# Performance work log

Hardware: AMD Instinct MI355X
Metric: run time of the kernel (lower is better)

Reference implementation:

```python
import jax, jax.numpy as jnp
import numpy as np

N_HEADS = 8
D_HEAD = 64
INNER = N_HEADS * D_HEAD  # 512
D_X = 512
D_CTX = 768

def setup_inputs() -> dict:
    key = jax.random.key(0)
    ks = jax.random.split(key, 7)
    x = jax.random.normal(ks[0], (4, 4096, D_X), dtype=jnp.float32)
    context = jax.random.normal(ks[1], (4, 1024, D_CTX), dtype=jnp.float32)
    # Glorot-ish scaled params
    Wq = jax.random.normal(ks[2], (D_X, INNER), dtype=jnp.float32) / np.sqrt(D_X)
    Wk = jax.random.normal(ks[3], (D_CTX, INNER), dtype=jnp.float32) / np.sqrt(D_CTX)
    Wv = jax.random.normal(ks[4], (D_CTX, INNER), dtype=jnp.float32) / np.sqrt(D_CTX)
    Wo = jax.random.normal(ks[5], (INNER, INNER), dtype=jnp.float32) / np.sqrt(INNER)
    bo = jnp.zeros((INNER,), dtype=jnp.float32)
    return {"x": x, "context": context, "Wq": Wq, "Wk": Wk, "Wv": Wv, "Wo": Wo, "bo": bo}

def reference(x, context, Wq, Wk, Wv, Wo, bo):
    B, Nq, _ = x.shape
    Nc = context.shape[1]
    scale = D_HEAD ** -0.5
    # QKV projections (no bias), reshape to heads: b s (h d) -> b h s d
    q = (x @ Wq).reshape(B, Nq, N_HEADS, D_HEAD).transpose(0, 2, 1, 3)
    k = (context @ Wk).reshape(B, Nc, N_HEADS, D_HEAD).transpose(0, 2, 1, 3)
    v = (context @ Wv).reshape(B, Nc, N_HEADS, D_HEAD).transpose(0, 2, 1, 3)
    # scores: [B, H, Nq, Nc]
    score = jnp.einsum('bhqd,bhkd->bhqk', q, k) * scale
    weights = jax.nn.softmax(score, axis=-1)
    attn = jnp.einsum('bhqk,bhkd->bhqd', weights, v)
    out = attn.transpose(0, 2, 1, 3).reshape(B, Nq, INNER)
    return out @ Wo + bo
```

## Files before the change

### kernel.cpp

```cpp
#include <hip/hip_runtime.h>
#include <math.h>

typedef __attribute__((ext_vector_type(8))) short s8v;
typedef __attribute__((ext_vector_type(4))) float f4v;
typedef unsigned short u16;
typedef unsigned int u32;

constexpr int Bsz = 4, NQ = 4096, NC = 1024, NH = 8, DH = 64, DI = 512, DC = 768;

__device__ __forceinline__ u16 f2bf(float f) {
  union { float f; u32 u; } v; v.f = f;
  u32 r = v.u + 0x7fff + ((v.u >> 16) & 1);
  return (u16)(r >> 16);
}

__device__ __forceinline__ u32 pack2(float a, float b) {
  union { float f; u32 u; } ua, ub; ua.f = a; ub.f = b;
#if __has_builtin(__builtin_amdgcn_perm)
  return __builtin_amdgcn_perm(ub.u + 0x8000u, ua.u + 0x8000u, 0x07060302u);
#else
  return ((ub.u + 0x8000u) & 0xffff0000u) | ((ua.u + 0x8000u) >> 16);
#endif
}

#if __has_builtin(__builtin_amdgcn_exp2f)
#define EXP2(x) __builtin_amdgcn_exp2f(x)
#else
#define EXP2(x) exp2f(x)
#endif

__device__ __forceinline__ void g2l16(const void* g, void* l) {
  __builtin_amdgcn_global_load_lds((const __attribute__((address_space(1))) u32*)g,
                                   (__attribute__((address_space(3))) u32*)l, 16, 0, 0);
}

__global__ __launch_bounds__(256) void prep(const float* __restrict__ x, const float* __restrict__ ctx,
                                            const float* __restrict__ Wq, const float* __restrict__ Wk,
                                            const float* __restrict__ Wv, const float* __restrict__ Wo,
                                            u16* __restrict__ xb, u16* __restrict__ cb,
                                            u16* __restrict__ wqT, u16* __restrict__ wkvT,
                                            u16* __restrict__ woT) {
  int bx = blockIdx.x;
  if (bx < 11264) {
    const int NX4 = Bsz * NQ * DI / 4;
    const int NC4 = Bsz * NC * DC / 4;
    int i = bx * 256 + threadIdx.x;
    float4 v; u16* dst; int j;
    if (i < NX4) { v = ((const float4*)x)[i]; dst = xb; j = i; }
    else { j = i - NX4; if (j >= NC4) return; v = ((const float4*)ctx)[j]; dst = cb; }
    ushort4 o; o.x = f2bf(v.x); o.y = f2bf(v.y); o.z = f2bf(v.z); o.w = f2bf(v.w);
    ((ushort4*)dst)[j] = o;
    return;
  }
  int idx = bx - 11264;
  int z = idx / 96, rem = idx % 96, kx = rem % 12, ny = rem / 12;
  const float* src; u16* dst; int K; const int N = 512;
  if (z == 0)      { src = Wq; dst = wqT;              K = 512; }
  else if (z == 1) { src = Wk; dst = wkvT;             K = 768; }
  else if (z == 2) { src = Wv; dst = wkvT + 512 * 768; K = 768; }
  else             { src = Wo; dst = woT;              K = 512; }
  int k0 = kx * 64, n0 = ny * 64;
  if (k0 >= K) return;
  __shared__ u16 t[64][65];
  int tid = threadIdx.x, jr = tid & 63, ir = tid >> 6;
  for (int it = 0; it < 16; ++it) { int i = it * 4 + ir; t[i][jr] = f2bf(src[(size_t)(k0 + i) * N + n0 + jr]); }
  __syncthreads();
  for (int it = 0; it < 16; ++it) { int i = it * 4 + ir; dst[(size_t)(n0 + i) * K + k0 + jr] = t[jr][i]; }
}

template <int MODE>
__device__ __forceinline__ void gemm_body(const u16* __restrict__ A, const u16* __restrict__ Bt,
                                          void* __restrict__ C0, void* __restrict__ C1,
                                          const float* __restrict__ bias, int N, int K,
                                          float oscale, int nbx, int mby,
                                          u16* Al, u16* Bl) {
  int mb = mby * 128, nb = nbx * 64;
  int tid = threadIdx.x, lane = tid & 63, quad = lane >> 4, l16 = lane & 15, wave = tid >> 6;
  int wm = (wave >> 1) * 64, wn = (wave & 1) * 32;
  f4v acc[4][2];
  #pragma unroll
  for (int i = 0; i < 4; i++)
    #pragma unroll
    for (int j = 0; j < 2; j++) acc[i][j] = (f4v){0.f, 0.f, 0.f, 0.f};

  int r0 = tid >> 2, c0 = (tid & 3) * 8;
  const u16* Ap0 = A + (size_t)(mb + r0) * K + c0;
  const u16* Ap1 = A + (size_t)(mb + r0 + 64) * K + c0;
  const u16* Bp0 = Bt + (size_t)(nb + r0) * K + c0;

#define GSTAGE(k0, buf) do { \
    u16* al_ = Al + (buf) * 4096; u16* bl_ = Bl + (buf) * 2048; \
    g2l16(Ap0 + (k0), al_ + tid * 8); \
    g2l16(Ap1 + (k0), al_ + (tid + 256) * 8); \
    g2l16(Bp0 + (k0), bl_ + tid * 8); } while (0)

  GSTAGE(0, 0);
  int nk = K >> 5;
  for (int t = 0; t < nk; ++t) {
    __syncthreads();
    if (t + 1 < nk) GSTAGE((t + 1) * 32, (t + 1) & 1);
    const u16* al = Al + (t & 1) * 4096;
    const u16* bl = Bl + (t & 1) * 2048;
    s8v af[4], bfr[2];
    #pragma unroll
    for (int i = 0; i < 4; i++) af[i] = *(const s8v*)(al + (wm + i * 16 + l16) * 32 + quad * 8);
    #pragma unroll
    for (int j = 0; j < 2; j++) bfr[j] = *(const s8v*)(bl + (wn + j * 16 + l16) * 32 + quad * 8);
    #pragma unroll
    for (int i = 0; i < 4; i++)
      #pragma unroll
      for (int j = 0; j < 2; j++)
        acc[i][j] = __builtin_amdgcn_mfma_f32_16x16x32_bf16(af[i], bfr[j], acc[i][j], 0, 0, 0);
  }
#undef GSTAGE
  #pragma unroll
  for (int i = 0; i < 4; i++) {
    int rbase = mb + wm + i * 16 + quad * 4;
    #pragma unroll
    for (int j = 0; j < 2; j++) {
      int col = nb + wn + j * 16 + l16;
      if (MODE == 0) {
        u16* Cb = (u16*)C0;
        #pragma unroll
        for (int r = 0; r < 4; r++) Cb[(size_t)(rbase + r) * N + col] = f2bf(acc[i][j][r] * oscale);
      } else if (MODE == 1) {
        float* Cf = (float*)C0;
        #pragma unroll
        for (int r = 0; r < 4; r++) Cf[(size_t)(rbase + r) * N + col] = acc[i][j][r] + bias[col];
      } else {
        if (nbx < 8) {
          u16* Kb = (u16*)C0;
          #pragma unroll
          for (int r = 0; r < 4; r++) Kb[(size_t)(rbase + r) * 512 + col] = f2bf(acc[i][j][r]);
        } else {
          u16* Vt = (u16*)C1;
          int hd = col - 512, h = hd >> 6, d = hd & 63;
          int bb = rbase >> 10, tl = rbase & 1023;
          int tbase = tl & ~63, a0 = tl & 63;
          int pb = (a0 & 32) + ((a0 & 15) >> 2) * 8 + (((a0 >> 4) & 1) << 2);
          uint2 ov;
          ov.x = pack2(acc[i][j][0], acc[i][j][1]);
          ov.y = pack2(acc[i][j][2], acc[i][j][3]);
          *(uint2*)(Vt + ((size_t)(bb * NH + h) * DH + d) * NC + tbase + pb) = ov;
        }
      }
    }
  }
}

__global__ __launch_bounds__(256, 4) void proj_all(const u16* __restrict__ xb, const u16* __restrict__ cb,
                                                   const u16* __restrict__ wqT, const u16* __restrict__ wkvT,
                                                   u16* __restrict__ Qb, u16* __restrict__ Kb,
                                                   u16* __restrict__ Vtb, float qscale) {
  __shared__ alignas(16) u16 Al[2][128][32];
  __shared__ alignas(16) u16 Bl[2][64][32];
  int bx = blockIdx.x;
  if (bx < 1024) {
    gemm_body<0>(xb, wqT, Qb, nullptr, nullptr, 512, 512, qscale, bx & 7, bx >> 3,
                 (u16*)Al, (u16*)Bl);
  } else {
    int bi = bx - 1024;
    gemm_body<2>(cb, wkvT, Kb, Vtb, nullptr, 1024, 768, 1.0f, bi & 15, bi >> 4,
                 (u16*)Al, (u16*)Bl);
  }
}

__global__ __launch_bounds__(256, 4) void outproj(const u16* __restrict__ Ob, const u16* __restrict__ woT,
                                                  float* __restrict__ out, const float* __restrict__ bo) {
  __shared__ alignas(16) u16 Al[2][128][32];
  __shared__ alignas(16) u16 Bl[2][64][32];
  gemm_body<1>(Ob, woT, out, nullptr, bo, 512, 512, 1.0f, blockIdx.x, blockIdx.y,
               (u16*)Al, (u16*)Bl);
}

__global__ __launch_bounds__(128, 2) void attn(const u16* __restrict__ Q, const u16* __restrict__ Kb,
                                               const u16* __restrict__ Vt, u16* __restrict__ O) {
  __shared__ alignas(16) u16 Kl[2][64][64];
  __shared__ alignas(16) u16 Vl[2][64][64];
  int qt = blockIdx.x, h = blockIdx.y, b = blockIdx.z;
  int tid = threadIdx.x, wave = tid >> 6, lane = tid & 63, quad = lane >> 4, l16 = lane & 15;
  int q0 = qt * 128 + wave * 64;
  int x7 = l16 & 7;

  int kr = tid >> 3, kc = (tid & 7) ^ (kr & 7);
  const u16* kg = Kb + ((size_t)b * NC + kr) * 512 + h * DH + kc * 8;
  const u16* vg = Vt + ((size_t)(b * NH + h) * DH + kr) * NC + kc * 8;

#define ASTAGE(kt, buf) do { \
    const u16* kg_ = kg + (size_t)(kt) * 64 * 512; \
    const u16* vg_ = vg + (kt) * 64; \
    u16* kl_ = (u16*)Kl + (buf) * 4096; u16* vl_ = (u16*)Vl + (buf) * 4096; \
    _Pragma("unroll") \
    for (int it = 0; it < 4; ++it) { \
      g2l16(kg_ + (size_t)it * 16 * 512, kl_ + (tid + it * 128) * 8); \
      g2l16(vg_ + (size_t)it * 16 * NC,  vl_ + (tid + it * 128) * 8); \
    } } while (0)

  s8v aq[4][2];
  {
    const u16* Qp = Q + ((size_t)b * NQ + q0 + l16) * DI + h * DH + quad * 8;
    #pragma unroll
    for (int n = 0; n < 4; n++) {
      aq[n][0] = *(const s8v*)(Qp + (size_t)n * 16 * DI);
      aq[n][1] = *(const s8v*)(Qp + (size_t)n * 16 * DI + 32);
    }
  }
  f4v oacc[4][4];
  float lsum[4] = {0.f, 0.f, 0.f, 0.f};
  #pragma unroll
  for (int d = 0; d < 4; d++)
    #pragma unroll
    for (int n = 0; n < 4; n++) oacc[d][n] = (f4v){0.f, 0.f, 0.f, 0.f};

  ASTAGE(0, 0);
  for (int kt = 0; kt < NC / 64; ++kt) {
    int buf = kt & 1;
    __syncthreads();
    if (kt + 1 < NC / 64) ASTAGE(kt + 1, buf ^ 1);
    const u16* kb = (const u16*)Kl + buf * 4096;
    const u16* vb = (const u16*)Vl + buf * 4096;

    #pragma unroll
    for (int c = 0; c < 2; c++) {
      f4v S[2][4];
      #pragma unroll
      for (int mi = 0; mi < 2; mi++)
        #pragma unroll
        for (int n = 0; n < 4; n++) S[mi][n] = (f4v){0.f, 0.f, 0.f, 0.f};
      #pragma unroll
      for (int cd = 0; cd < 2; cd++) {
        int rA = 32 * c + l16;
        int ch = ((4 * cd + quad) ^ x7) * 8;
        s8v kf0 = *(const s8v*)(kb + rA * 64 + ch);
        s8v kf1 = *(const s8v*)(kb + (rA + 16) * 64 + ch);
        #pragma unroll
        for (int n = 0; n < 4; n++) {
          S[0][n] = __builtin_amdgcn_mfma_f32_16x16x32_bf16(kf0, aq[n][cd], S[0][n], 0, 0, 0);
          S[1][n] = __builtin_amdgcn_mfma_f32_16x16x32_bf16(kf1, aq[n][cd], S[1][n], 0, 0, 0);
        }
      }
      s8v pf[4];
      #pragma unroll
      for (int n = 0; n < 4; n++) {
        float p00 = EXP2(S[0][n][0]), p01 = EXP2(S[0][n][1]), p02 = EXP2(S[0][n][2]), p03 = EXP2(S[0][n][3]);
        float p10 = EXP2(S[1][n][0]), p11 = EXP2(S[1][n][1]), p12 = EXP2(S[1][n][2]), p13 = EXP2(S[1][n][3]);
        lsum[n] += (p00 + p01) + (p02 + p03) + (p10 + p11) + (p12 + p13);
        union { u32 d[4]; s8v v; } u;
        u.d[0] = pack2(p00, p01); u.d[1] = pack2(p02, p03);
        u.d[2] = pack2(p10, p11); u.d[3] = pack2(p12, p13);
        pf[n] = u.v;
      }
      #pragma unroll
      for (int d = 0; d < 4; d++) {
        int rV = d * 16 + l16;
        int ch = ((4 * c + quad) ^ x7) * 8;
        s8v vf = *(const s8v*)(vb + rV * 64 + ch);
        #pragma unroll
        for (int n = 0; n < 4; n++)
          oacc[d][n] = __builtin_amdgcn_mfma_f32_16x16x32_bf16(vf, pf[n], oacc[d][n], 0, 0, 0);
      }
    }
  }
#undef ASTAGE

  float inv[4];
  #pragma unroll
  for (int n = 0; n < 4; n++) {
    float s = lsum[n];
    s += __shfl_xor(s, 16); s += __shfl_xor(s, 32);
    inv[n] = 1.0f / s;
  }
  #pragma unroll
  for (int d = 0; d < 4; d++)
    #pragma unroll
    for (int n = 0; n < 4; n++) {
      int q = q0 + n * 16 + l16;
      uint2 ov;
      ov.x = pack2(oacc[d][n][0] * inv[n], oacc[d][n][1] * inv[n]);
      ov.y = pack2(oacc[d][n][2] * inv[n], oacc[d][n][3] * inv[n]);
      *(uint2*)(O + ((size_t)b * NQ + q) * DI + h * DH + d * 16 + quad * 4) = ov;
    }
}

extern "C" void kernel_launch(void* const* d_in, const int* in_sizes, int n_in,
                              void* d_out, int out_size, void* d_ws, size_t ws_size,
                              hipStream_t stream) {
  const float* x   = (const float*)d_in[0];
  const float* ctx = (const float*)d_in[1];
  const float* Wq  = (const float*)d_in[2];
  const float* Wk  = (const float*)d_in[3];
  const float* Wv  = (const float*)d_in[4];
  const float* Wo  = (const float*)d_in[5];
  const float* bo  = (const float*)d_in[6];
  float* out = (float*)d_out;

  u16* w    = (u16*)d_ws;
  u16* xb   = w;
  u16* cb   = xb   + 8388608;
  u16* wqT  = cb   + 3145728;
  u16* wkvT = wqT  + 262144;
  u16* woT  = wkvT + 786432;
  u16* Qb   = woT  + 262144;
  u16* Kbuf = Qb   + 8388608;
  u16* Vtb  = Kbuf + 2097152;
  u16* Ob   = Vtb  + 2097152;

  const float qscale = 0.125f * 1.44269504f;

  prep<<<11648, 256, 0, stream>>>(x, ctx, Wq, Wk, Wv, Wo, xb, cb, wqT, wkvT, woT);
  proj_all<<<1536, 256, 0, stream>>>(xb, cb, wqT, wkvT, Qb, Kbuf, Vtb, qscale);
  attn<<<dim3(32, 8, 4), 128, 0, stream>>>(Qb, Kbuf, Vtb, Ob);
  outproj<<<dim3(8, 128), 256, 0, stream>>>(Ob, woT, out, bo);
}
```

Baseline: 207.5 us.

## Widen projection GEMM tiles to 128x128 and shrink attention KV tiles to 32

The shared GEMM body now computes 128x128 output tiles, with each wave holding a 64x64 accumulator block. This halves the block count for the projection and output GEMMs and increases operand reuse per LDS load. The attention kernel streams K/V in 32-key tiles instead of 64, which halves its shared memory per block and raises the occupancy hint from 2 to 4 blocks per CU. The trade-offs are more accumulator registers and lower occupancy in the GEMMs, and twice as many barriers and load iterations in the attention loop.

```diff
diff --git a/kernel.cpp b/kernel.cpp
--- a/kernel.cpp
+++ b/kernel.cpp
@@ -74,25 +74,27 @@
                                           const float* __restrict__ bias, int N, int K,
                                           float oscale, int nbx, int mby,
                                           u16* Al, u16* Bl) {
-  int mb = mby * 128, nb = nbx * 64;
+  int mb = mby * 128, nb = nbx * 128;
   int tid = threadIdx.x, lane = tid & 63, quad = lane >> 4, l16 = lane & 15, wave = tid >> 6;
-  int wm = (wave >> 1) * 64, wn = (wave & 1) * 32;
-  f4v acc[4][2];
+  int wm = (wave >> 1) * 64, wn = (wave & 1) * 64;
+  f4v acc[4][4];
   #pragma unroll
   for (int i = 0; i < 4; i++)
     #pragma unroll
-    for (int j = 0; j < 2; j++) acc[i][j] = (f4v){0.f, 0.f, 0.f, 0.f};
+    for (int j = 0; j < 4; j++) acc[i][j] = (f4v){0.f, 0.f, 0.f, 0.f};
 
   int r0 = tid >> 2, c0 = (tid & 3) * 8;
   const u16* Ap0 = A + (size_t)(mb + r0) * K + c0;
   const u16* Ap1 = A + (size_t)(mb + r0 + 64) * K + c0;
   const u16* Bp0 = Bt + (size_t)(nb + r0) * K + c0;
+  const u16* Bp1 = Bt + (size_t)(nb + r0 + 64) * K + c0;
 
 #define GSTAGE(k0, buf) do { \
-    u16* al_ = Al + (buf) * 4096; u16* bl_ = Bl + (buf) * 2048; \
+    u16* al_ = Al + (buf) * 4096; u16* bl_ = Bl + (buf) * 4096; \
     g2l16(Ap0 + (k0), al_ + tid * 8); \
     g2l16(Ap1 + (k0), al_ + (tid + 256) * 8); \
-    g2l16(Bp0 + (k0), bl_ + tid * 8); } while (0)
+    g2l16(Bp0 + (k0), bl_ + tid * 8); \
+    g2l16(Bp1 + (k0), bl_ + (tid + 256) * 8); } while (0)
 
   GSTAGE(0, 0);
   int nk = K >> 5;
@@ -100,16 +102,16 @@
     __syncthreads();
     if (t + 1 < nk) GSTAGE((t + 1) * 32, (t + 1) & 1);
     const u16* al = Al + (t & 1) * 4096;
-    const u16* bl = Bl + (t & 1) * 2048;
-    s8v af[4], bfr[2];
+    const u16* bl = Bl + (t & 1) * 4096;
+    s8v af[4], bfr[4];
     #pragma unroll
     for (int i = 0; i < 4; i++) af[i] = *(const s8v*)(al + (wm + i * 16 + l16) * 32 + quad * 8);
     #pragma unroll
-    for (int j = 0; j < 2; j++) bfr[j] = *(const s8v*)(bl + (wn + j * 16 + l16) * 32 + quad * 8);
+    for (int j = 0; j < 4; j++) bfr[j] = *(const s8v*)(bl + (wn + j * 16 + l16) * 32 + quad * 8);
     #pragma unroll
     for (int i = 0; i < 4; i++)
       #pragma unroll
-      for (int j = 0; j < 2; j++)
+      for (int j = 0; j < 4; j++)
         acc[i][j] = __builtin_amdgcn_mfma_f32_16x16x32_bf16(af[i], bfr[j], acc[i][j], 0, 0, 0);
   }
 #undef GSTAGE
@@ -117,7 +119,7 @@
   for (int i = 0; i < 4; i++) {
     int rbase = mb + wm + i * 16 + quad * 4;
     #pragma unroll
-    for (int j = 0; j < 2; j++) {
+    for (int j = 0; j < 4; j++) {
       int col = nb + wn + j * 16 + l16;
       if (MODE == 0) {
         u16* Cb = (u16*)C0;
@@ -128,7 +130,7 @@
         #pragma unroll
         for (int r = 0; r < 4; r++) Cf[(size_t)(rbase + r) * N + col] = acc[i][j][r] + bias[col];
       } else {
-        if (nbx < 8) {
+        if (col < 512) {
           u16* Kb = (u16*)C0;
           #pragma unroll
           for (int r = 0; r < 4; r++) Kb[(size_t)(rbase + r) * 512 + col] = f2bf(acc[i][j][r]);
@@ -148,35 +150,35 @@
   }
 }
 
-__global__ __launch_bounds__(256, 4) void proj_all(const u16* __restrict__ xb, const u16* __restrict__ cb,
+__global__ __launch_bounds__(256, 3) void proj_all(const u16* __restrict__ xb, const u16* __restrict__ cb,
                                                    const u16* __restrict__ wqT, const u16* __restrict__ wkvT,
                                                    u16* __restrict__ Qb, u16* __restrict__ Kb,
                                                    u16* __restrict__ Vtb, float qscale) {
   __shared__ alignas(16) u16 Al[2][128][32];
-  __shared__ alignas(16) u16 Bl[2][64][32];
+  __shared__ alignas(16) u16 Bl[2][128][32];
   int bx = blockIdx.x;
-  if (bx < 1024) {
-    gemm_body<0>(xb, wqT, Qb, nullptr, nullptr, 512, 512, qscale, bx & 7, bx >> 3,
+  if (bx < 512) {
+    gemm_body<0>(xb, wqT, Qb, nullptr, nullptr, 512, 512, qscale, bx & 3, bx >> 2,
                  (u16*)Al, (u16*)Bl);
   } else {
-    int bi = bx - 1024;
-    gemm_body<2>(cb, wkvT, Kb, Vtb, nullptr, 1024, 768, 1.0f, bi & 15, bi >> 4,
+    int bi = bx - 512;
+    gemm_body<2>(cb, wkvT, Kb, Vtb, nullptr, 1024, 768, 1.0f, bi & 7, bi >> 3,
                  (u16*)Al, (u16*)Bl);
   }
 }
 
-__global__ __launch_bounds__(256, 4) void outproj(const u16* __restrict__ Ob, const u16* __restrict__ woT,
+__global__ __launch_bounds__(256, 2) void outproj(const u16* __restrict__ Ob, const u16* __restrict__ woT,
                                                   float* __restrict__ out, const float* __restrict__ bo) {
   __shared__ alignas(16) u16 Al[2][128][32];
-  __shared__ alignas(16) u16 Bl[2][64][32];
+  __shared__ alignas(16) u16 Bl[2][128][32];
   gemm_body<1>(Ob, woT, out, nullptr, bo, 512, 512, 1.0f, blockIdx.x, blockIdx.y,
                (u16*)Al, (u16*)Bl);
 }
 
-__global__ __launch_bounds__(128, 2) void attn(const u16* __restrict__ Q, const u16* __restrict__ Kb,
+__global__ __launch_bounds__(128, 4) void attn(const u16* __restrict__ Q, const u16* __restrict__ Kb,
                                                const u16* __restrict__ Vt, u16* __restrict__ O) {
-  __shared__ alignas(16) u16 Kl[2][64][64];
-  __shared__ alignas(16) u16 Vl[2][64][64];
+  __shared__ alignas(16) u16 Kl[2][32][64];
+  __shared__ alignas(16) u16 Vl[2][64][32];
   int qt = blockIdx.x, h = blockIdx.y, b = blockIdx.z;
   int tid = threadIdx.x, wave = tid >> 6, lane = tid & 63, quad = lane >> 4, l16 = lane & 15;
   int q0 = qt * 128 + wave * 64;
@@ -184,17 +186,17 @@
 
   int kr = tid >> 3, kc = (tid & 7) ^ (kr & 7);
   const u16* kg = Kb + ((size_t)b * NC + kr) * 512 + h * DH + kc * 8;
-  const u16* vg = Vt + ((size_t)(b * NH + h) * DH + kr) * NC + kc * 8;
+  int vr = tid >> 2, vc = tid & 3;
+  const u16* vg = Vt + ((size_t)(b * NH + h) * DH + vr) * NC + vc * 8;
 
 #define ASTAGE(kt, buf) do { \
-    const u16* kg_ = kg + (size_t)(kt) * 64 * 512; \
-    const u16* vg_ = vg + (kt) * 64; \
-    u16* kl_ = (u16*)Kl + (buf) * 4096; u16* vl_ = (u16*)Vl + (buf) * 4096; \
-    _Pragma("unroll") \
-    for (int it = 0; it < 4; ++it) { \
-      g2l16(kg_ + (size_t)it * 16 * 512, kl_ + (tid + it * 128) * 8); \
-      g2l16(vg_ + (size_t)it * 16 * NC,  vl_ + (tid + it * 128) * 8); \
-    } } while (0)
+    const u16* kg_ = kg + (size_t)(kt) * 32 * 512; \
+    const u16* vg_ = vg + (kt) * 32; \
+    u16* kl_ = (u16*)Kl + (buf) * 2048; u16* vl_ = (u16*)Vl + (buf) * 2048; \
+    g2l16(kg_,            kl_ + tid * 8); \
+    g2l16(kg_ + 16 * 512, kl_ + (tid + 128) * 8); \
+    g2l16(vg_,            vl_ + tid * 8); \
+    g2l16(vg_ + 32 * NC,  vl_ + (tid + 128) * 8); } while (0)
 
   s8v aq[4][2];
   {
@@ -213,52 +215,46 @@
     for (int n = 0; n < 4; n++) oacc[d][n] = (f4v){0.f, 0.f, 0.f, 0.f};
 
   ASTAGE(0, 0);
-  for (int kt = 0; kt < NC / 64; ++kt) {
+  for (int kt = 0; kt < NC / 32; ++kt) {
     int buf = kt & 1;
     __syncthreads();
-    if (kt + 1 < NC / 64) ASTAGE(kt + 1, buf ^ 1);
-    const u16* kb = (const u16*)Kl + buf * 4096;
-    const u16* vb = (const u16*)Vl + buf * 4096;
-
-    #pragma unroll
-    for (int c = 0; c < 2; c++) {
-      f4v S[2][4];
+    if (kt + 1 < NC / 32) ASTAGE(kt + 1, buf ^ 1);
+    const u16* kb = (const u16*)Kl + buf * 2048;
+    const u16* vb = (const u16*)Vl + buf * 2048;
+
+    f4v S[2][4];
+    #pragma unroll
+    for (int mi = 0; mi < 2; mi++)
       #pragma unroll
-      for (int mi = 0; mi < 2; mi++)
-        #pragma unroll
-        for (int n = 0; n < 4; n++) S[mi][n] = (f4v){0.f, 0.f, 0.f, 0.f};
-      #pragma unroll
-      for (int cd = 0; cd < 2; cd++) {
-        int rA = 32 * c + l16;
-        int ch = ((4 * cd + quad) ^ x7) * 8;
-        s8v kf0 = *(const s8v*)(kb + rA * 64 + ch);
-        s8v kf1 = *(const s8v*)(kb + (rA + 16) * 64 + ch);
-        #pragma unroll
-        for (int n = 0; n < 4; n++) {
-          S[0][n] = __builtin_amdgcn_mfma_f32_16x16x32_bf16(kf0, aq[n][cd], S[0][n], 0, 0, 0);
-          S[1][n] = __builtin_amdgcn_mfma_f32_16x16x32_bf16(kf1, aq[n][cd], S[1][n], 0, 0, 0);
-        }
-      }
-      s8v pf[4];
+      for (int n = 0; n < 4; n++) S[mi][n] = (f4v){0.f, 0.f, 0.f, 0.f};
+    #pragma unroll
+    for (int cd = 0; cd < 2; cd++) {
+      int ch = ((4 * cd + quad) ^ x7) * 8;
+      s8v kf0 = *(const s8v*)(kb + l16 * 64 + ch);
+      s8v kf1 = *(const s8v*)(kb + (l16 + 16) * 64 + ch);
       #pragma unroll
       for (int n = 0; n < 4; n++) {
-        float p00 = EXP2(S[0][n][0]), p01 = EXP2(S[0][n][1]), p02 = EXP2(S[0][n][2]), p03 = EXP2(S[0][n][3]);
-        float p10 = EXP2(S[1][n][0]), p11 = EXP2(S[1][n][1]), p12 = EXP2(S[1][n][2]), p13 = EXP2(S[1][n][3]);
-        lsum[n] += (p00 + p01) + (p02 + p03) + (p10 + p11) + (p12 + p13);
-        union { u32 d[4]; s8v v; } u;
-        u.d[0] = pack2(p00, p01); u.d[1] = pack2(p02, p03);
-        u.d[2] = pack2(p10, p11); u.d[3] = pack2(p12, p13);
-        pf[n] = u.v;
+        S[0][n] = __builtin_amdgcn_mfma_f32_16x16x32_bf16(kf0, aq[n][cd], S[0][n], 0, 0, 0);
+        S[1][n] = __builtin_amdgcn_mfma_f32_16x16x32_bf16(kf1, aq[n][cd], S[1][n], 0, 0, 0);
       }
+    }
+    s8v pf[4];
+    #pragma unroll
+    for (int n = 0; n < 4; n++) {
+      float p00 = EXP2(S[0][n][0]), p01 = EXP2(S[0][n][1]), p02 = EXP2(S[0][n][2]), p03 = EXP2(S[0][n][3]);
+      float p10 = EXP2(S[1][n][0]), p11 = EXP2(S[1][n][1]), p12 = EXP2(S[1][n][2]), p13 = EXP2(S[1][n][3]);
+      lsum[n] += (p00 + p01) + (p02 + p03) + (p10 + p11) + (p12 + p13);
+      union { u32 d[4]; s8v v; } u;
+      u.d[0] = pack2(p00, p01); u.d[1] = pack2(p02, p03);
+      u.d[2] = pack2(p10, p11); u.d[3] = pack2(p12, p13);
+      pf[n] = u.v;
+    }
+    #pragma unroll
+    for (int d = 0; d < 4; d++) {
+      s8v vf = *(const s8v*)(vb + (d * 16 + l16) * 32 + quad * 8);
       #pragma unroll
-      for (int d = 0; d < 4; d++) {
-        int rV = d * 16 + l16;
-        int ch = ((4 * c + quad) ^ x7) * 8;
-        s8v vf = *(const s8v*)(vb + rV * 64 + ch);
-        #pragma unroll
-        for (int n = 0; n < 4; n++)
-          oacc[d][n] = __builtin_amdgcn_mfma_f32_16x16x32_bf16(vf, pf[n], oacc[d][n], 0, 0, 0);
-      }
+      for (int n = 0; n < 4; n++)
+        oacc[d][n] = __builtin_amdgcn_mfma_f32_16x16x32_bf16(vf, pf[n], oacc[d][n], 0, 0, 0);
     }
   }
 #undef ASTAGE
@@ -308,7 +304,7 @@
   const float qscale = 0.125f * 1.44269504f;
 
   prep<<<11648, 256, 0, stream>>>(x, ctx, Wq, Wk, Wv, Wo, xb, cb, wqT, wkvT, woT);
-  proj_all<<<1536, 256, 0, stream>>>(xb, cb, wqT, wkvT, Qb, Kbuf, Vtb, qscale);
+  proj_all<<<768, 256, 0, stream>>>(xb, cb, wqT, wkvT, Qb, Kbuf, Vtb, qscale);
   attn<<<dim3(32, 8, 4), 128, 0, stream>>>(Qb, Kbuf, Vtb, Ob);
-  outproj<<<dim3(8, 128), 256, 0, stream>>>(Ob, woT, out, bo);
-}
+  outproj<<<dim3(4, 128), 256, 0, stream>>>(Ob, woT, out, bo);
+}
```

Measured after the change: 253.5 us. 1.22x slower.
